# Kernel optimization log

Hardware: AMD Instinct MI355X
Metric: run time of the kernel (lower is better)

## Reference

```python
import jax, jax.numpy as jnp
import numpy as np

S, B, D, H = 1024, 16, 512, 8
DH = D // H  # 64


def setup_inputs() -> dict:
    key = jax.random.key(0)
    k1, k2, k3, k4, k5 = jax.random.split(key, 5)
    x = jax.random.normal(k1, (S, B, D), dtype=jnp.float32)
    # binary validity mask [B, S]: 1 = keep, 0 = masked out (matches torch usage)
    mask = (jax.random.uniform(k2, (B, S)) > 0.2).astype(jnp.float32)
    scale = 1.0 / np.sqrt(D)
    wq = jax.random.normal(k3, (H, DH, D), dtype=jnp.float32) * scale
    wk = jax.random.normal(k4, (H, DH, D), dtype=jnp.float32) * scale
    wv = jax.random.normal(k5, (H, DH, D), dtype=jnp.float32) * scale
    return {"x": x, "mask": mask, "wq": wq, "wk": wk, "wv": wv}


def reference(x, mask, wq, wk, wv):
    # x: [S, B, D]; mask: [B, S]; w*: [H, DH, D] (stacked bias-free Linear weights)
    dh = wq.shape[1]
    # per-hop projections for all hops at once (Linear: y = x @ W.T)
    q = jnp.einsum('sbd,hed->bhse', x, wq)  # [B,H,S,DH]
    k = jnp.einsum('sbd,hed->bhse', x, wk)
    v = jnp.einsum('sbd,hed->bhse', x, wv)
    scores = jnp.einsum('bhse,bhte->bhst', q, k)  # [B,H,S,S]
    inv_mask = (1.0 - mask)[:, None, None, :]      # broadcast over heads, query pos
    align = jnp.tanh(scores / jnp.sqrt(jnp.asarray(dh, x.dtype))) - 10000.0 * inv_mask
    align = jax.nn.softmax(align, axis=-1)
    out = jnp.einsum('bhst,bhte->bhse', align, v)  # [B,H,S,DH]
    s, b = x.shape[0], x.shape[1]
    # concat hops along feature dim, back to seq-first: [S, B, H*DH]
    return jnp.transpose(out, (2, 0, 1, 3)).reshape(s, b, -1)
```

## Files before the change

### kernel.cpp

```cpp
#include <hip/hip_runtime.h>
#include <stdint.h>
#include <stddef.h>

#define SS 1024
#define BB 16
#define DD 512
#define HH 8
#define DHH 64

typedef __attribute__((ext_vector_type(8))) short bf16x8;
typedef __attribute__((ext_vector_type(4))) float f32x4;
typedef __attribute__((ext_vector_type(16))) float f32x16;
typedef __attribute__((ext_vector_type(4))) float float4v;
typedef __attribute__((ext_vector_type(2))) float float2v;
typedef __attribute__((ext_vector_type(4))) unsigned short us4;

__device__ __forceinline__ unsigned short f2bf(float f) {
  union { float f; unsigned int u; } v; v.f = f;
  unsigned int x = v.u;
  return (unsigned short)((x + 0x7FFFu + ((x >> 16) & 1u)) >> 16);
}

#define GLDS16(dst, src)                                                                  \
  __builtin_amdgcn_global_load_lds(                                                      \
      (const __attribute__((address_space(1))) unsigned int*)(const void*)(src),         \
      (__attribute__((address_space(3))) unsigned int*)(void*)(dst), 16, 0, 0)

__global__ void cvt_kernel(const float* __restrict__ x,
                           const float* __restrict__ wq,
                           const float* __restrict__ wk,
                           const float* __restrict__ wv,
                           unsigned short* __restrict__ xb,
                           unsigned short* __restrict__ wb) {
  const int i = blockIdx.x * 256 + threadIdx.x;
  const int n_x4 = (SS * BB * DD) / 4;
  if (i < n_x4) {
    float4v v = ((const float4v*)x)[i];
    us4 o;
    o[0] = f2bf(v[0]); o[1] = f2bf(v[1]); o[2] = f2bf(v[2]); o[3] = f2bf(v[3]);
    ((us4*)xb)[i] = o;
  } else {
    const int j = i - n_x4;
    const int sel = j >> 16;
    const int off4 = j & 65535;
    const float* wsrc = (sel == 0) ? wq : ((sel == 1) ? wk : wv);
    const float scale = (sel == 0) ? 0.36067376022224085f : 1.0f;
    float4v v = ((const float4v*)wsrc)[off4];
    us4 o;
    o[0] = f2bf(v[0] * scale); o[1] = f2bf(v[1] * scale);
    o[2] = f2bf(v[2] * scale); o[3] = f2bf(v[3] * scale);
    ((us4*)wb)[(sel << 16) + off4] = o;
  }
}

__global__ __launch_bounds__(256) void proj_kernel(
    const unsigned short* __restrict__ xb,
    const unsigned short* __restrict__ wb,
    unsigned short* __restrict__ qb,
    unsigned short* __restrict__ kb,
    unsigned short* __restrict__ vt) {
  const int bm = blockIdx.x * 128;
  const int bn = blockIdx.y * 128;
  const int b = blockIdx.z / 3;
  const int wsel = blockIdx.z % 3;

  __shared__ unsigned short At[128 * 32];
  __shared__ unsigned short Bt[128 * 32];
  __shared__ unsigned short OT[4][64 * 72];

  const int tid = threadIdx.x;
  const int w = tid >> 6;
  const int lane = tid & 63;

  const unsigned short* wptr = wb + wsel * (512 * DD);

  f32x4 acc[4][4];
#pragma unroll
  for (int mi = 0; mi < 4; ++mi)
#pragma unroll
    for (int ni = 0; ni < 4; ++ni) acc[mi][ni] = (f32x4){0.f, 0.f, 0.f, 0.f};

  const int m0 = (w & 1) * 64;
  const int n0 = (w >> 1) * 64;

  for (int kt = 0; kt < 16; ++kt) {
#pragma unroll
    for (int i = 0; i < 2; ++i) {
      const int idx8 = i * 256 + tid;
      const int r = idx8 >> 2;
      const int c8 = idx8 & 3;
      GLDS16(&At[(i * 256 + w * 64) * 8],
             xb + (size_t)(bm + r) * (BB * DD) + b * DD + kt * 32 + c8 * 8);
      GLDS16(&Bt[(i * 256 + w * 64) * 8],
             wptr + (size_t)(bn + r) * DD + kt * 32 + c8 * 8);
    }
    __syncthreads();
    bf16x8 af[4], bfr[4];
#pragma unroll
    for (int mi = 0; mi < 4; ++mi)
      af[mi] = *(const bf16x8*)&At[(m0 + mi * 16 + (lane & 15)) * 32 + (lane >> 4) * 8];
#pragma unroll
    for (int ni = 0; ni < 4; ++ni)
      bfr[ni] = *(const bf16x8*)&Bt[(n0 + ni * 16 + (lane & 15)) * 32 + (lane >> 4) * 8];
#pragma unroll
    for (int mi = 0; mi < 4; ++mi)
#pragma unroll
      for (int ni = 0; ni < 4; ++ni)
        acc[mi][ni] =
            __builtin_amdgcn_mfma_f32_16x16x32_bf16(af[mi], bfr[ni], acc[mi][ni], 0, 0, 0);
    __syncthreads();
  }

  const int h = (bn + n0) >> 6;
  unsigned short* OTw = &OT[w][0];
  if (wsel != 2) {
#pragma unroll
    for (int mi = 0; mi < 4; ++mi)
#pragma unroll
      for (int ni = 0; ni < 4; ++ni)
#pragma unroll
        for (int j = 0; j < 4; ++j)
          OTw[(mi * 16 + (lane >> 4) * 4 + j) * 72 + ni * 16 + (lane & 15)] =
              f2bf(acc[mi][ni][j]);
  } else {
#pragma unroll
    for (int mi = 0; mi < 4; ++mi)
#pragma unroll
      for (int ni = 0; ni < 4; ++ni) {
        us4 pk;
#pragma unroll
        for (int j = 0; j < 4; ++j) pk[j] = f2bf(acc[mi][ni][j]);
        *(us4*)&OTw[(ni * 16 + (lane & 15)) * 72 + mi * 16 + (lane >> 4) * 4] = pk;
      }
  }
  unsigned short* gout = (wsel == 0) ? qb : ((wsel == 1) ? kb : vt);
#pragma unroll
  for (int pass = 0; pass < 8; ++pass) {
    const int row = pass * 8 + (lane >> 3);
    bf16x8 vrow = *(const bf16x8*)&OTw[row * 72 + (lane & 7) * 8];
    size_t dst;
    if (wsel != 2)
      dst = ((size_t)(b * HH + h) * SS + (size_t)(bm + m0 + row)) * DHH + (lane & 7) * 8;
    else
      dst = ((size_t)(b * HH + h) * DHH + (size_t)row) * SS + (bm + m0) + (lane & 7) * 8;
    *(bf16x8*)&gout[dst] = vrow;
  }
}

__global__ __launch_bounds__(512, 4) void attn_kernel(
    const unsigned short* __restrict__ qb,
    const unsigned short* __restrict__ kb,
    const unsigned short* __restrict__ vt,
    const float* __restrict__ mask,
    float* __restrict__ out) {
  const int id = blockIdx.x;
  const int xcd = id & 7;
  const int slot = id >> 3;
  const int bh = xcd * 16 + (slot >> 2);
  const int qt = slot & 3;
  const int b = bh >> 3;
  const int h = bh & 7;
  const int tid = threadIdx.x;
  const int w = tid >> 6;
  const int lane = tid & 63;
  const int l31 = lane & 31;
  const int hi32 = lane >> 5;

  __shared__ float mask_s[SS];
  __shared__ unsigned short Ks[2][64 * 64];
  __shared__ unsigned short Vs[2][64 * 64];
  __shared__ float rs_s[8][32];

  {
    float2v mv = *(const float2v*)&mask[b * SS + tid * 2];
    mask_s[tid * 2] = mv[0];
    mask_s[tid * 2 + 1] = mv[1];
  }

  const size_t base_qk = (size_t)bh * SS * DHH;
  const int q0 = qt * 256 + w * 32;

  bf16x8 aq[4];
  {
    const unsigned short* qp = qb + base_qk + (size_t)(q0 + l31) * DHH + hi32 * 8;
    aq[0] = *(const bf16x8*)(qp);
    aq[1] = *(const bf16x8*)(qp + 16);
    aq[2] = *(const bf16x8*)(qp + 32);
    aq[3] = *(const bf16x8*)(qp + 48);
  }

  const int srow = w * 8 + (lane >> 3);
  const int sxb = ((lane & 7) << 4) ^ ((srow & 7) << 4);
  const unsigned short* ksrc = kb + base_qk + (size_t)srow * DHH + (sxb >> 1);
  const unsigned short* vsrc = vt + (size_t)bh * DHH * SS + (size_t)srow * SS + (sxb >> 1);

#define STAGE(bb, kt2)                                                    \
  do {                                                                    \
    GLDS16(&Ks[bb][w * 512], ksrc + (size_t)(kt2) * (64 * DHH));          \
    GLDS16(&Vs[bb][w * 512], vsrc + (size_t)(kt2) * 64);                  \
  } while (0)

  STAGE(0, 0);

  f32x16 accO[2];
#pragma unroll
  for (int n = 0; n < 2; ++n)
#pragma unroll
    for (int i = 0; i < 16; ++i) accO[n][i] = 0.f;
  float rs = 0.f;

  __syncthreads();

  int buf = 0;
  for (int kt = 0; kt < 16; ++kt) {
    if (kt < 15) STAGE(buf ^ 1, kt + 1);
    const char* Kb = (const char*)&Ks[buf][0];
    const char* Vb = (const char*)&Vs[buf][0];
    const int k0 = kt * 64;

#pragma unroll
    for (int T = 0; T < 2; ++T) {
      const int krow = T * 32 + l31;
      const int ksw = (krow & 7) << 4;
      f32x16 sc = {};
#pragma unroll
      for (int ks = 0; ks < 4; ++ks) {
        bf16x8 kf = *(const bf16x8*)(Kb + krow * 128 + ((ks * 32 + hi32 * 16) ^ ksw));
        sc = __builtin_amdgcn_mfma_f32_32x32x16_bf16(kf, aq[ks], sc, 0, 0, 0);
      }
      unsigned int pu[16];
#pragma unroll
      for (int g = 0; g < 4; ++g) {
        float4v mv = *(const float4v*)&mask_s[k0 + T * 32 + g * 8 + hi32 * 4];
#pragma unroll
        for (int i = 0; i < 4; ++i) {
          float u = __builtin_amdgcn_exp2f(sc[g * 4 + i]);
          float r = __builtin_amdgcn_rcpf(1.f + u);
          float p = mv[i] * __builtin_amdgcn_exp2f(-2.88539008178f * r);
          rs += p;
          union { float f; unsigned int u; } cv;
          cv.f = p;
          pu[g * 4 + i] = cv.u;
        }
      }
      unsigned int wv[8];
#pragma unroll
      for (int m = 0; m < 8; ++m)
        wv[m] = __builtin_amdgcn_perm(pu[2 * m + 1], pu[2 * m], 0x07060302u);
      unsigned int t0 = hi32 ? wv[0] : wv[2];
      unsigned int t1 = hi32 ? wv[1] : wv[3];
      unsigned int t2 = hi32 ? wv[4] : wv[6];
      unsigned int t3 = hi32 ? wv[5] : wv[7];
      unsigned int s0 = (unsigned int)__shfl_xor((int)t0, 32, 64);
      unsigned int s1 = (unsigned int)__shfl_xor((int)t1, 32, 64);
      unsigned int s2 = (unsigned int)__shfl_xor((int)t2, 32, 64);
      unsigned int s3 = (unsigned int)__shfl_xor((int)t3, 32, 64);
      union { unsigned int u[4]; bf16x8 v; } f0, f1;
      f0.u[0] = hi32 ? s0 : wv[0];
      f0.u[1] = hi32 ? s1 : wv[1];
      f0.u[2] = hi32 ? wv[2] : s0;
      f0.u[3] = hi32 ? wv[3] : s1;
      f1.u[0] = hi32 ? s2 : wv[4];
      f1.u[1] = hi32 ? s3 : wv[5];
      f1.u[2] = hi32 ? wv[6] : s2;
      f1.u[3] = hi32 ? wv[7] : s3;
#pragma unroll
      for (int n = 0; n < 2; ++n) {
        const int vrow = n * 32 + l31;
        const int vsw = (vrow & 7) << 4;
        bf16x8 bv0 = *(const bf16x8*)(Vb + vrow * 128 + (((T * 2 + 0) * 32 + hi32 * 16) ^ vsw));
        bf16x8 bv1 = *(const bf16x8*)(Vb + vrow * 128 + (((T * 2 + 1) * 32 + hi32 * 16) ^ vsw));
        accO[n] = __builtin_amdgcn_mfma_f32_32x32x16_bf16(f0.v, bv0, accO[n], 0, 0, 0);
        accO[n] = __builtin_amdgcn_mfma_f32_32x32x16_bf16(f1.v, bv1, accO[n], 0, 0, 0);
      }
    }
    __syncthreads();
    buf ^= 1;
  }
#undef STAGE

  rs += __shfl_xor(rs, 32, 64);
  if (hi32 == 0) rs_s[w][l31] = __builtin_amdgcn_rcpf(rs);
  float4v ri[4];
#pragma unroll
  for (int g = 0; g < 4; ++g) ri[g] = *(const float4v*)&rs_s[w][g * 8 + hi32 * 4];

#pragma unroll
  for (int n = 0; n < 2; ++n)
#pragma unroll
    for (int g = 0; g < 4; ++g)
#pragma unroll
      for (int i = 0; i < 4; ++i) {
        const int qrow = q0 + g * 8 + hi32 * 4 + i;
        out[((size_t)qrow * BB + b) * DD + h * DHH + n * 32 + l31] =
            accO[n][g * 4 + i] * ri[g][i];
      }
}

extern "C" void kernel_launch(void* const* d_in, const int* in_sizes, int n_in,
                              void* d_out, int out_size, void* d_ws, size_t ws_size,
                              hipStream_t stream) {
  const float* x = (const float*)d_in[0];
  const float* mask = (const float*)d_in[1];
  const float* wq = (const float*)d_in[2];
  const float* wk = (const float*)d_in[3];
  const float* wv = (const float*)d_in[4];
  float* out = (float*)d_out;

  char* ws = (char*)d_ws;
  unsigned short* xb = (unsigned short*)(ws);
  unsigned short* wb = (unsigned short*)(ws + (16ull << 20));
  unsigned short* qb = (unsigned short*)(ws + (18ull << 20));
  unsigned short* kb = (unsigned short*)(ws + (34ull << 20));
  unsigned short* vt = (unsigned short*)(ws + (50ull << 20));

  cvt_kernel<<<dim3(8960), 256, 0, stream>>>(x, wq, wk, wv, xb, wb);
  proj_kernel<<<dim3(8, 4, 48), 256, 0, stream>>>(xb, wb, qb, kb, vt);
  attn_kernel<<<dim3(512), 512, 0, stream>>>(qb, kb, vt, mask, out);
}
```

Baseline: 115.2 us.

## Shrink attention blocks to 256 threads, single-buffer K/V, precompute additive mask

The attention kernel moves from 512-thread blocks with double-buffered K/V and a per-block mask copy in LDS to 256-thread blocks (1024 blocks, 8 per CU) with single-buffered K/V tiles. The mask is turned once, in the convert kernel, into an additive log-domain bias that is folded into the exp2 argument with an fma and read straight from global memory. The aim is more resident blocks per CU and less LDS and ALU work per element. In exchange, loads are no longer prefetched under compute, so each tile now waits on a load plus barrier and relies on other blocks to hide that latency.

```diff
diff --git a/kernel.cpp b/kernel.cpp
--- a/kernel.cpp
+++ b/kernel.cpp
@@ -12,7 +12,6 @@
 typedef __attribute__((ext_vector_type(4))) float f32x4;
 typedef __attribute__((ext_vector_type(16))) float f32x16;
 typedef __attribute__((ext_vector_type(4))) float float4v;
-typedef __attribute__((ext_vector_type(2))) float float2v;
 typedef __attribute__((ext_vector_type(4))) unsigned short us4;
 
 __device__ __forceinline__ unsigned short f2bf(float f) {
@@ -30,16 +29,19 @@
                            const float* __restrict__ wq,
                            const float* __restrict__ wk,
                            const float* __restrict__ wv,
+                           const float* __restrict__ mask,
                            unsigned short* __restrict__ xb,
-                           unsigned short* __restrict__ wb) {
+                           unsigned short* __restrict__ wb,
+                           float* __restrict__ maskq) {
   const int i = blockIdx.x * 256 + threadIdx.x;
   const int n_x4 = (SS * BB * DD) / 4;
+  const int n_w4 = 3 * 65536;
   if (i < n_x4) {
     float4v v = ((const float4v*)x)[i];
     us4 o;
     o[0] = f2bf(v[0]); o[1] = f2bf(v[1]); o[2] = f2bf(v[2]); o[3] = f2bf(v[3]);
     ((us4*)xb)[i] = o;
-  } else {
+  } else if (i < n_x4 + n_w4) {
     const int j = i - n_x4;
     const int sel = j >> 16;
     const int off4 = j & 65535;
@@ -50,6 +52,13 @@
     o[0] = f2bf(v[0] * scale); o[1] = f2bf(v[1] * scale);
     o[2] = f2bf(v[2] * scale); o[3] = f2bf(v[3] * scale);
     ((us4*)wb)[(sel << 16) + off4] = o;
+  } else {
+    const int j = i - n_x4 - n_w4;
+    float4v mv = ((const float4v*)mask)[j];
+    float4v o;
+#pragma unroll
+    for (int c = 0; c < 4; ++c) o[c] = (mv[c] > 0.5f) ? 0.f : -16384.f;
+    ((float4v*)maskq)[j] = o;
   }
 }
 
@@ -147,17 +156,17 @@
   }
 }
 
-__global__ __launch_bounds__(512, 4) void attn_kernel(
+__global__ __launch_bounds__(256, 8) void attn_kernel(
     const unsigned short* __restrict__ qb,
     const unsigned short* __restrict__ kb,
     const unsigned short* __restrict__ vt,
-    const float* __restrict__ mask,
+    const float* __restrict__ maskq,
     float* __restrict__ out) {
   const int id = blockIdx.x;
   const int xcd = id & 7;
   const int slot = id >> 3;
-  const int bh = xcd * 16 + (slot >> 2);
-  const int qt = slot & 3;
+  const int bh = xcd * 16 + (slot >> 3);
+  const int qt = slot & 7;
   const int b = bh >> 3;
   const int h = bh & 7;
   const int tid = threadIdx.x;
@@ -166,19 +175,12 @@
   const int l31 = lane & 31;
   const int hi32 = lane >> 5;
 
-  __shared__ float mask_s[SS];
-  __shared__ unsigned short Ks[2][64 * 64];
-  __shared__ unsigned short Vs[2][64 * 64];
-  __shared__ float rs_s[8][32];
-
-  {
-    float2v mv = *(const float2v*)&mask[b * SS + tid * 2];
-    mask_s[tid * 2] = mv[0];
-    mask_s[tid * 2 + 1] = mv[1];
-  }
+  __shared__ unsigned short Ks[64 * 64];
+  __shared__ unsigned short Vs[64 * 64];
+  __shared__ float rs_s[4][32];
 
   const size_t base_qk = (size_t)bh * SS * DHH;
-  const int q0 = qt * 256 + w * 32;
+  const int q0 = qt * 128 + w * 32;
 
   bf16x8 aq[4];
   {
@@ -189,18 +191,21 @@
     aq[3] = *(const bf16x8*)(qp + 48);
   }
 
-  const int srow = w * 8 + (lane >> 3);
-  const int sxb = ((lane & 7) << 4) ^ ((srow & 7) << 4);
-  const unsigned short* ksrc = kb + base_qk + (size_t)srow * DHH + (sxb >> 1);
-  const unsigned short* vsrc = vt + (size_t)bh * DHH * SS + (size_t)srow * SS + (sxb >> 1);
-
-#define STAGE(bb, kt2)                                                    \
+  const int sr0 = w * 16 + (lane >> 3);
+  const int sxb = (((lane & 7) ^ (lane >> 3)) << 4);
+  const unsigned short* ksrc0 = kb + base_qk + (size_t)sr0 * DHH + (sxb >> 1);
+  const unsigned short* ksrc1 = ksrc0 + 8 * DHH;
+  const unsigned short* vsrc0 =
+      vt + (size_t)bh * DHH * SS + (size_t)sr0 * SS + (sxb >> 1);
+  const unsigned short* vsrc1 = vsrc0 + 8 * SS;
+
+#define STAGE(kt2)                                                        \
   do {                                                                    \
-    GLDS16(&Ks[bb][w * 512], ksrc + (size_t)(kt2) * (64 * DHH));          \
-    GLDS16(&Vs[bb][w * 512], vsrc + (size_t)(kt2) * 64);                  \
+    GLDS16(&Ks[(w * 16) * 64], ksrc0 + (size_t)(kt2) * (64 * DHH));       \
+    GLDS16(&Ks[(w * 16 + 8) * 64], ksrc1 + (size_t)(kt2) * (64 * DHH));   \
+    GLDS16(&Vs[(w * 16) * 64], vsrc0 + (size_t)(kt2) * 64);               \
+    GLDS16(&Vs[(w * 16 + 8) * 64], vsrc1 + (size_t)(kt2) * 64);           \
   } while (0)
-
-  STAGE(0, 0);
 
   f32x16 accO[2];
 #pragma unroll
@@ -208,15 +213,11 @@
 #pragma unroll
     for (int i = 0; i < 16; ++i) accO[n][i] = 0.f;
   float rs = 0.f;
-
-  __syncthreads();
-
-  int buf = 0;
+  const float* mrow = maskq + b * SS;
+
   for (int kt = 0; kt < 16; ++kt) {
-    if (kt < 15) STAGE(buf ^ 1, kt + 1);
-    const char* Kb = (const char*)&Ks[buf][0];
-    const char* Vb = (const char*)&Vs[buf][0];
-    const int k0 = kt * 64;
+    STAGE(kt);
+    __syncthreads();
 
 #pragma unroll
     for (int T = 0; T < 2; ++T) {
@@ -225,18 +226,19 @@
       f32x16 sc = {};
 #pragma unroll
       for (int ks = 0; ks < 4; ++ks) {
-        bf16x8 kf = *(const bf16x8*)(Kb + krow * 128 + ((ks * 32 + hi32 * 16) ^ ksw));
+        bf16x8 kf = *(const bf16x8*)((const char*)Ks + krow * 128 +
+                                     ((ks * 32 + hi32 * 16) ^ ksw));
         sc = __builtin_amdgcn_mfma_f32_32x32x16_bf16(kf, aq[ks], sc, 0, 0, 0);
       }
       unsigned int pu[16];
 #pragma unroll
       for (int g = 0; g < 4; ++g) {
-        float4v mv = *(const float4v*)&mask_s[k0 + T * 32 + g * 8 + hi32 * 4];
+        float4v mv = *(const float4v*)&mrow[kt * 64 + T * 32 + g * 8 + hi32 * 4];
 #pragma unroll
         for (int i = 0; i < 4; ++i) {
           float u = __builtin_amdgcn_exp2f(sc[g * 4 + i]);
           float r = __builtin_amdgcn_rcpf(1.f + u);
-          float p = mv[i] * __builtin_amdgcn_exp2f(-2.88539008178f * r);
+          float p = __builtin_amdgcn_exp2f(__builtin_fmaf(r, -2.88539008178f, mv[i]));
           rs += p;
           union { float f; unsigned int u; } cv;
           cv.f = p;
@@ -268,14 +270,15 @@
       for (int n = 0; n < 2; ++n) {
         const int vrow = n * 32 + l31;
         const int vsw = (vrow & 7) << 4;
-        bf16x8 bv0 = *(const bf16x8*)(Vb + vrow * 128 + (((T * 2 + 0) * 32 + hi32 * 16) ^ vsw));
-        bf16x8 bv1 = *(const bf16x8*)(Vb + vrow * 128 + (((T * 2 + 1) * 32 + hi32 * 16) ^ vsw));
+        bf16x8 bv0 = *(const bf16x8*)((const char*)Vs + vrow * 128 +
+                                      (((T * 2 + 0) * 32 + hi32 * 16) ^ vsw));
+        bf16x8 bv1 = *(const bf16x8*)((const char*)Vs + vrow * 128 +
+                                      (((T * 2 + 1) * 32 + hi32 * 16) ^ vsw));
         accO[n] = __builtin_amdgcn_mfma_f32_32x32x16_bf16(f0.v, bv0, accO[n], 0, 0, 0);
         accO[n] = __builtin_amdgcn_mfma_f32_32x32x16_bf16(f1.v, bv1, accO[n], 0, 0, 0);
       }
     }
     __syncthreads();
-    buf ^= 1;
   }
 #undef STAGE
 
@@ -310,11 +313,12 @@
   char* ws = (char*)d_ws;
   unsigned short* xb = (unsigned short*)(ws);
   unsigned short* wb = (unsigned short*)(ws + (16ull << 20));
+  float* maskq = (float*)(ws + (17ull << 20) + (512ull << 10));
   unsigned short* qb = (unsigned short*)(ws + (18ull << 20));
   unsigned short* kb = (unsigned short*)(ws + (34ull << 20));
   unsigned short* vt = (unsigned short*)(ws + (50ull << 20));
 
-  cvt_kernel<<<dim3(8960), 256, 0, stream>>>(x, wq, wk, wv, xb, wb);
+  cvt_kernel<<<dim3(8976), 256, 0, stream>>>(x, wq, wk, wv, mask, xb, wb, maskq);
   proj_kernel<<<dim3(8, 4, 48), 256, 0, stream>>>(xb, wb, qb, kb, vt);
-  attn_kernel<<<dim3(512), 512, 0, stream>>>(qb, kb, vt, mask, out);
-}
+  attn_kernel<<<dim3(1024), 256, 0, stream>>>(qb, kb, vt, maskq, out);
+}
```

Result: slower. 282.9 us (+145.6%).
